# Optimization experiments

Hardware: AMD Instinct MI355X
Metric: run time of the kernel (lower is better)

Reference implementation:

```python
import jax, jax.numpy as jnp
import numpy as np

N, E, G = 30000, 480000, 64
IN, H, L = 24, 512, 6


def setup_inputs() -> dict:
    key = jax.random.key(0)
    ks = jax.random.split(key, 20)
    s = 0.05
    inp = {
        "x": jax.random.normal(ks[0], (N, IN), dtype=jnp.float32),
        "edge_index": jax.random.randint(ks[1], (2, E), 0, N, dtype=jnp.int64),
        "batch": jnp.sort(jax.random.randint(ks[2], (N,), 0, G, dtype=jnp.int64)),
        # node encoder
        "enc_w": jax.random.normal(ks[3], (IN, H), dtype=jnp.float32) * s,
        "enc_b": jnp.zeros((H,), dtype=jnp.float32),
        # per-layer message MLP (stacked over L layers), weights stored [in, out]
        "mlp_w1": jax.random.normal(ks[4], (L, H, H), dtype=jnp.float32) * s,
        "mlp_b1": jnp.zeros((L, H), dtype=jnp.float32),
        "mlp_w2": jax.random.normal(ks[5], (L, H, H), dtype=jnp.float32) * s,
        "mlp_b2": jnp.zeros((L, H), dtype=jnp.float32),
        # per-layer GRUCell params, [in, 3H] layout (gates order: r, z, n)
        "gru_wih": jax.random.normal(ks[6], (L, H, 3 * H), dtype=jnp.float32) * s,
        "gru_whh": jax.random.normal(ks[7], (L, H, 3 * H), dtype=jnp.float32) * s,
        "gru_bih": jnp.zeros((L, 3 * H), dtype=jnp.float32),
        "gru_bhh": jnp.zeros((L, 3 * H), dtype=jnp.float32),
        # head MLP
        "head_w1": jax.random.normal(ks[8], (H, H // 2), dtype=jnp.float32) * s,
        "head_b1": jnp.zeros((H // 2,), dtype=jnp.float32),
        "head_w2": jax.random.normal(ks[9], (H // 2, 1), dtype=jnp.float32) * s,
        "head_b2": jnp.zeros((1,), dtype=jnp.float32),
    }
    return inp


def _forward(x, edge_index, batch, enc_w, enc_b, mlp_w1, mlp_b1, mlp_w2, mlp_b2,
             gru_wih, gru_whh, gru_bih, gru_bhh, head_w1, head_b1, head_w2, head_b2):
    src, dst = edge_index[0], edge_index[1]
    h = x @ enc_w + enc_b  # [N, H]
    for l in range(L):
        # message MLP depends only on x_j, so compute per-node then gather
        msg = jnp.maximum(h @ mlp_w1[l] + mlp_b1[l], 0.0) @ mlp_w2[l] + mlp_b2[l]  # [N, H]
        # scatter-add over edges + self-loop contribution (add_self_loops)
        m = jax.ops.segment_sum(msg[src], dst, num_segments=N) + msg  # [N, H]
        # GRUCell(input=m, hidden=h); torch gate order: reset, update, new
        gi = m @ gru_wih[l] + gru_bih[l]
        gh = h @ gru_whh[l] + gru_bhh[l]
        r = jax.nn.sigmoid(gi[:, :H] + gh[:, :H])
        z = jax.nn.sigmoid(gi[:, H:2 * H] + gh[:, H:2 * H])
        n = jnp.tanh(gi[:, 2 * H:] + r * gh[:, 2 * H:])
        h = (1.0 - z) * n + z * h
    # global mean pool per graph
    sums = jax.ops.segment_sum(h, batch, num_segments=G)
    cnt = jax.ops.segment_sum(jnp.ones((N,), dtype=h.dtype), batch, num_segments=G)
    pooled = sums / jnp.maximum(cnt, 1.0)[:, None]  # [G, H]
    out = jnp.maximum(pooled @ head_w1 + head_b1, 0.0) @ head_w2 + head_b2
    return out[:, 0]  # [G]


def reference(x, edge_index, batch, enc_w, enc_b, mlp_w1, mlp_b1, mlp_w2, mlp_b2,
              gru_wih, gru_whh, gru_bih, gru_bhh, head_w1, head_b1, head_w2, head_b2):
    return _forward(x, edge_index, batch, enc_w, enc_b, mlp_w1, mlp_b1, mlp_w2, mlp_b2,
                    gru_wih, gru_whh, gru_bih, gru_bhh, head_w1, head_b1, head_w2, head_b2)
```

## Files before the change

### kernel.cpp

```cpp
#include <hip/hip_runtime.h>
#include <hip/hip_bf16.h>
#include <math.h>

#define N_NODES 30000
#define N_EDGES 480000
#define N_GRAPH 64
#define DIN 24
#define HD 512
#define NL 6

typedef __hip_bfloat16 bf16;
using short8 = __attribute__((ext_vector_type(8))) short;
using f32x4 = __attribute__((ext_vector_type(4))) float;

#define ASYNC16(gp, lp)                                              \
    __builtin_amdgcn_global_load_lds(                                \
        (const __attribute__((address_space(1))) void*)(gp),         \
        (__attribute__((address_space(3))) void*)(lp), 16, 0, 0)

__device__ __forceinline__ float sigmoidf_(float x) { return 1.0f / (1.0f + expf(-x)); }
__device__ __forceinline__ float b2f(unsigned short u) {
    return __uint_as_float(((unsigned int)u) << 16);
}
__device__ __forceinline__ unsigned short f2b(float f) {
    bf16 b = __float2bfloat16(f);
    return *(unsigned short*)&b;
}

__global__ __launch_bounds__(256) void enc_kernel(const float* __restrict__ x,
                                                  const float* __restrict__ w,
                                                  const float* __restrict__ b,
                                                  bf16* __restrict__ h) {
    __shared__ float xs[DIN];
    int row = blockIdx.x;
    int tid = threadIdx.x;
    if (tid < DIN) xs[tid] = x[row * DIN + tid];
    __syncthreads();
    for (int c = tid; c < HD; c += 256) {
        float acc = b[c];
#pragma unroll
        for (int k = 0; k < DIN; k++) acc = fmaf(xs[k], w[k * HD + c], acc);
        h[(size_t)row * HD + c] = __float2bfloat16(acc);
    }
}

__global__ __launch_bounds__(256) void twcvt_kernel(const float* __restrict__ W,
                                                    bf16* __restrict__ WtH,
                                                    bf16* __restrict__ WtL, int Nc) {
    __shared__ float s[32][33];
    int l = blockIdx.z;
    const float* Wp = W + (size_t)l * HD * Nc;
    size_t ob = (size_t)l * HD * Nc;
    int k0 = blockIdx.y * 32, c0 = blockIdx.x * 32;
    int tx = threadIdx.x & 31, ty = threadIdx.x >> 5;
    for (int r = ty; r < 32; r += 8) s[r][tx] = Wp[(size_t)(k0 + r) * Nc + c0 + tx];
    __syncthreads();
    for (int r = ty; r < 32; r += 8) {
        float v = s[tx][r];
        unsigned short hu = f2b(v);
        float hf = b2f(hu);
        size_t o = ob + (size_t)(c0 + r) * HD + k0 + tx;
        *(unsigned short*)&WtH[o] = hu;
        WtL[o] = __float2bfloat16(v - hf);
    }
}

template <bool RELU>
__global__ __launch_bounds__(256) void gemm_mfma(const bf16* __restrict__ A,
                                                 const bf16* __restrict__ WtH,
                                                 const bf16* __restrict__ WtL,
                                                 const float* __restrict__ bias,
                                                 bf16* __restrict__ C, int n) {
    __shared__ bf16 As[128 * 32];
    __shared__ bf16 BH[128 * 32];
    __shared__ bf16 BL[128 * 32];
    int tid = threadIdx.x;
    int wv = tid >> 6, lane = tid & 63;
    int quad = lane >> 4, l16 = lane & 15;
    int crow = lane >> 2, cseg = lane & 3;
    int gseg = cseg ^ ((crow >> 1) & 3);
    int fsw = (quad ^ ((l16 >> 1) & 3)) * 8;
    int row0 = blockIdx.y * 128, col0 = blockIdx.x * 128;
    f32x4 acc[2][8] = {};

    int aoff[4], alds[4];
    int boff[8];
    const bf16* wb = (wv == 2) ? WtH : WtL;
    bf16* bdst = (wv == 2) ? BH : BL;
    if (wv < 2) {
#pragma unroll
        for (int j = 0; j < 4; j++) {
            int ch = wv * 4 + j;
            int gr = row0 + ch * 16 + crow;
            if (gr > n - 1) gr = n - 1;
            aoff[j] = gr * HD + gseg * 8;
            alds[j] = ch * 512;
        }
    } else {
#pragma unroll
        for (int s = 0; s < 8; s++) boff[s] = (col0 + s * 16 + crow) * HD + gseg * 8;
    }

    for (int kt = 0; kt < 512; kt += 32) {
        if (wv < 2) {
#pragma unroll
            for (int j = 0; j < 4; j++) ASYNC16(&A[aoff[j] + kt], &As[alds[j]]);
        } else {
#pragma unroll
            for (int s = 0; s < 8; s++) ASYNC16(&wb[boff[s] + kt], &bdst[s * 512]);
        }
        __syncthreads();
        short8 af[2];
#pragma unroll
        for (int i = 0; i < 2; i++)
            af[i] = *(const short8*)&As[(wv * 32 + i * 16 + l16) * 32 + fsw];
#pragma unroll
        for (int t = 0; t < 8; t++) {
            int fo = (t * 16 + l16) * 32 + fsw;
            short8 bh = *(const short8*)&BH[fo];
            short8 bl = *(const short8*)&BL[fo];
#pragma unroll
            for (int i = 0; i < 2; i++) {
                acc[i][t] = __builtin_amdgcn_mfma_f32_16x16x32_bf16(af[i], bh, acc[i][t], 0, 0, 0);
                acc[i][t] = __builtin_amdgcn_mfma_f32_16x16x32_bf16(af[i], bl, acc[i][t], 0, 0, 0);
            }
        }
        __syncthreads();
    }
#pragma unroll
    for (int t = 0; t < 8; t++) {
        int col = col0 + t * 16 + l16;
        float bb = bias[col];
#pragma unroll
        for (int i = 0; i < 2; i++) {
#pragma unroll
            for (int r = 0; r < 4; r++) {
                int row = row0 + wv * 32 + i * 16 + quad * 4 + r;
                if (row < n) {
                    float v = acc[i][t][r] + bb;
                    if (RELU) v = fmaxf(v, 0.0f);
                    C[(size_t)row * HD + col] = __float2bfloat16(v);
                }
            }
        }
    }
}

__global__ __launch_bounds__(256, 2) void gru_mfma(const bf16* __restrict__ M,
                                                   const bf16* __restrict__ Hc,
                                                   const bf16* __restrict__ WiH,
                                                   const bf16* __restrict__ WiL,
                                                   const bf16* __restrict__ WhH,
                                                   const bf16* __restrict__ WhL,
                                                   const float* __restrict__ bih,
                                                   const float* __restrict__ bhh,
                                                   bf16* __restrict__ Hn, int n) {
    __shared__ bf16 Ms[128 * 32];
    __shared__ bf16 Hs[128 * 32];
    __shared__ bf16 Ws[12 * 64 * 32];
    int tid = threadIdx.x;
    int wv = tid >> 6, lane = tid & 63;
    int quad = lane >> 4, l16 = lane & 15;
    int crow = lane >> 2, cseg = lane & 3;
    int gseg = cseg ^ ((crow >> 1) & 3);
    int fsw = (quad ^ ((l16 >> 1) & 3)) * 8;
    int row0 = blockIdx.y * 128, col0 = blockIdx.x * 64;
    f32x4 aR[2][4] = {}, aZ[2][4] = {}, aI[2][4] = {}, aHn[2][4] = {};

    int moff[8];
    const bf16* wgp[4];
    int wlds[4];
    if (wv == 0) {
#pragma unroll
        for (int j = 0; j < 8; j++) {
            int gr = row0 + j * 16 + crow;
            if (gr > n - 1) gr = n - 1;
            moff[j] = gr * HD + gseg * 8;
        }
    } else {
        const bf16* wbase[4] = {WiH, WiL, WhH, WhL};
#pragma unroll
        for (int pp = 0; pp < 4; pp++) {
            int p = (wv - 1) * 4 + pp;
            int mat = (p >= 6);
            int q = p - mat * 6;
            int g = q >> 1, pl = q & 1;
            const bf16* base = wbase[mat * 2 + pl] + (size_t)(g * HD + col0) * HD;
            wgp[pp] = base + crow * HD + gseg * 8;
            wlds[pp] = p * 2048;
        }
    }

    for (int kt = 0; kt < 512; kt += 32) {
        if (wv == 0) {
#pragma unroll
            for (int j = 0; j < 8; j++) {
                ASYNC16(&M[moff[j] + kt], &Ms[j * 512]);
                ASYNC16(&Hc[moff[j] + kt], &Hs[j * 512]);
            }
        } else {
#pragma unroll
            for (int pp = 0; pp < 4; pp++)
#pragma unroll
                for (int s = 0; s < 4; s++)
                    ASYNC16(wgp[pp] + (size_t)s * 16 * HD + kt, &Ws[wlds[pp] + s * 512]);
        }
        __syncthreads();
        short8 am[2], ah[2];
#pragma unroll
        for (int i = 0; i < 2; i++) {
            am[i] = *(const short8*)&Ms[(wv * 32 + i * 16 + l16) * 32 + fsw];
            ah[i] = *(const short8*)&Hs[(wv * 32 + i * 16 + l16) * 32 + fsw];
        }
#pragma unroll
        for (int t = 0; t < 4; t++) {
            int fo = (t * 16 + l16) * 32 + fsw;
            short8 wrh = *(const short8*)&Ws[0 * 2048 + fo];
            short8 wrl = *(const short8*)&Ws[1 * 2048 + fo];
            short8 wzh = *(const short8*)&Ws[2 * 2048 + fo];
            short8 wzl = *(const short8*)&Ws[3 * 2048 + fo];
            short8 wnh = *(const short8*)&Ws[4 * 2048 + fo];
            short8 wnl = *(const short8*)&Ws[5 * 2048 + fo];
            short8 vrh = *(const short8*)&Ws[6 * 2048 + fo];
            short8 vrl = *(const short8*)&Ws[7 * 2048 + fo];
            short8 vzh = *(const short8*)&Ws[8 * 2048 + fo];
            short8 vzl = *(const short8*)&Ws[9 * 2048 + fo];
            short8 vnh = *(const short8*)&Ws[10 * 2048 + fo];
            short8 vnl = *(const short8*)&Ws[11 * 2048 + fo];
#pragma unroll
            for (int i = 0; i < 2; i++) {
                aR[i][t] = __builtin_amdgcn_mfma_f32_16x16x32_bf16(am[i], wrh, aR[i][t], 0, 0, 0);
                aR[i][t] = __builtin_amdgcn_mfma_f32_16x16x32_bf16(am[i], wrl, aR[i][t], 0, 0, 0);
                aR[i][t] = __builtin_amdgcn_mfma_f32_16x16x32_bf16(ah[i], vrh, aR[i][t], 0, 0, 0);
                aR[i][t] = __builtin_amdgcn_mfma_f32_16x16x32_bf16(ah[i], vrl, aR[i][t], 0, 0, 0);
                aZ[i][t] = __builtin_amdgcn_mfma_f32_16x16x32_bf16(am[i], wzh, aZ[i][t], 0, 0, 0);
                aZ[i][t] = __builtin_amdgcn_mfma_f32_16x16x32_bf16(am[i], wzl, aZ[i][t], 0, 0, 0);
                aZ[i][t] = __builtin_amdgcn_mfma_f32_16x16x32_bf16(ah[i], vzh, aZ[i][t], 0, 0, 0);
                aZ[i][t] = __builtin_amdgcn_mfma_f32_16x16x32_bf16(ah[i], vzl, aZ[i][t], 0, 0, 0);
                aI[i][t] = __builtin_amdgcn_mfma_f32_16x16x32_bf16(am[i], wnh, aI[i][t], 0, 0, 0);
                aI[i][t] = __builtin_amdgcn_mfma_f32_16x16x32_bf16(am[i], wnl, aI[i][t], 0, 0, 0);
                aHn[i][t] = __builtin_amdgcn_mfma_f32_16x16x32_bf16(ah[i], vnh, aHn[i][t], 0, 0, 0);
                aHn[i][t] = __builtin_amdgcn_mfma_f32_16x16x32_bf16(ah[i], vnl, aHn[i][t], 0, 0, 0);
            }
        }
        __syncthreads();
    }
    const unsigned short* hp = (const unsigned short*)Hc;
#pragma unroll
    for (int t = 0; t < 4; t++) {
        int col = col0 + t * 16 + l16;
        float brz = bih[col] + bhh[col];
        float bzz = bih[HD + col] + bhh[HD + col];
        float bin_ = bih[2 * HD + col];
        float bhn_ = bhh[2 * HD + col];
#pragma unroll
        for (int i = 0; i < 2; i++) {
#pragma unroll
            for (int r = 0; r < 4; r++) {
                int row = row0 + wv * 32 + i * 16 + quad * 4 + r;
                if (row < n) {
                    float rg = sigmoidf_(aR[i][t][r] + brz);
                    float zg = sigmoidf_(aZ[i][t][r] + bzz);
                    float ng = tanhf(aI[i][t][r] + bin_ + rg * (aHn[i][t][r] + bhn_));
                    float hold = b2f(hp[(size_t)row * HD + col]);
                    Hn[(size_t)row * HD + col] = __float2bfloat16((1.0f - zg) * ng + zg * hold);
                }
            }
        }
    }
}

__global__ __launch_bounds__(256) void deg_kernel(const int* __restrict__ dst,
                                                  int* __restrict__ deg) {
    int e = blockIdx.x * 256 + threadIdx.x;
    if (e < N_EDGES) atomicAdd(&deg[dst[e]], 1);
}

__global__ __launch_bounds__(1024) void scan_kernel(const int* __restrict__ deg,
                                                    int* __restrict__ offs) {
    __shared__ int buf[1024];
    __shared__ int carry_s;
    int tid = threadIdx.x;
    if (tid == 0) carry_s = 0;
    __syncthreads();
    for (int base = 0; base < N_NODES; base += 1024) {
        int v = (base + tid < N_NODES) ? deg[base + tid] : 0;
        buf[tid] = v;
        __syncthreads();
        for (int s = 1; s < 1024; s <<= 1) {
            int t = (tid >= s) ? buf[tid - s] : 0;
            __syncthreads();
            buf[tid] += t;
            __syncthreads();
        }
        int incl = buf[tid];
        if (base + tid < N_NODES) offs[base + tid] = carry_s + incl - v;
        __syncthreads();
        if (tid == 0) carry_s += buf[1023];
        __syncthreads();
    }
    if (tid == 0) offs[N_NODES] = carry_s;
}

__global__ __launch_bounds__(256) void bucket_kernel(const int* __restrict__ src,
                                                     const int* __restrict__ dst,
                                                     const int* __restrict__ offs,
                                                     int* __restrict__ cursor,
                                                     unsigned short* __restrict__ elist) {
    int e = blockIdx.x * 256 + threadIdx.x;
    if (e >= N_EDGES) return;
    int d = dst[e];
    int pos = atomicAdd(&cursor[d], 1);
    elist[offs[d] + pos] = (unsigned short)src[e];
}

__global__ __launch_bounds__(256) void gather_kernel(const bf16* __restrict__ msg,
                                                     bf16* __restrict__ m,
                                                     const unsigned short* __restrict__ elist,
                                                     const int* __restrict__ offs) {
    int nid = blockIdx.x, tid = threadIdx.x;
    int beg = offs[nid], end = offs[nid + 1];
    const unsigned int* mp = (const unsigned int*)msg;
    unsigned int u = mp[(size_t)nid * 256 + tid];
    float ax = b2f((unsigned short)(u & 0xffffu));
    float ay = b2f((unsigned short)(u >> 16));
    int e = beg;
    for (; e + 3 < end; e += 4) {
        unsigned int v0 = mp[(size_t)elist[e] * 256 + tid];
        unsigned int v1 = mp[(size_t)elist[e + 1] * 256 + tid];
        unsigned int v2 = mp[(size_t)elist[e + 2] * 256 + tid];
        unsigned int v3 = mp[(size_t)elist[e + 3] * 256 + tid];
        ax += b2f((unsigned short)(v0 & 0xffffu)) + b2f((unsigned short)(v1 & 0xffffu)) +
              b2f((unsigned short)(v2 & 0xffffu)) + b2f((unsigned short)(v3 & 0xffffu));
        ay += b2f((unsigned short)(v0 >> 16)) + b2f((unsigned short)(v1 >> 16)) +
              b2f((unsigned short)(v2 >> 16)) + b2f((unsigned short)(v3 >> 16));
    }
    for (; e < end; e++) {
        unsigned int v0 = mp[(size_t)elist[e] * 256 + tid];
        ax += b2f((unsigned short)(v0 & 0xffffu));
        ay += b2f((unsigned short)(v0 >> 16));
    }
    unsigned int out = ((unsigned int)f2b(ay) << 16) | (unsigned int)f2b(ax);
    ((unsigned int*)m)[(size_t)nid * 256 + tid] = out;
}

__global__ __launch_bounds__(256) void pool_kernel(const bf16* __restrict__ h,
                                                   const int* __restrict__ batch,
                                                   float* __restrict__ pooled,
                                                   float* __restrict__ cnt) {
    int g = blockIdx.x;
    int col = blockIdx.y * 256 + threadIdx.x;
    int lo = 0, hi = N_NODES;
    while (lo < hi) { int mid = (lo + hi) >> 1; if (batch[mid] < g) lo = mid + 1; else hi = mid; }
    int gs = lo;
    hi = N_NODES;
    while (lo < hi) { int mid = (lo + hi) >> 1; if (batch[mid] < g + 1) lo = mid + 1; else hi = mid; }
    int ge = lo;
    const unsigned short* hp = (const unsigned short*)h;
    float acc = 0.0f;
    int r = gs;
    for (; r + 3 < ge; r += 4) {
        acc += b2f(hp[(size_t)r * HD + col]) + b2f(hp[(size_t)(r + 1) * HD + col]) +
               b2f(hp[(size_t)(r + 2) * HD + col]) + b2f(hp[(size_t)(r + 3) * HD + col]);
    }
    for (; r < ge; r++) acc += b2f(hp[(size_t)r * HD + col]);
    pooled[g * HD + col] = acc;
    if (blockIdx.y == 0 && threadIdx.x == 0) cnt[g] = (float)(ge - gs);
}

__global__ __launch_bounds__(256) void head_kernel(const float* __restrict__ pooled,
                                                   const float* __restrict__ cnt,
                                                   const float* __restrict__ w1,
                                                   const float* __restrict__ b1,
                                                   const float* __restrict__ w2,
                                                   const float* __restrict__ b2,
                                                   float* __restrict__ out) {
    __shared__ float prow[HD];
    __shared__ float red[256];
    int g = blockIdx.x, tid = threadIdx.x;
    float c = fmaxf(cnt[g], 1.0f);
    for (int j = tid; j < HD; j += 256) prow[j] = pooled[g * HD + j] / c;
    __syncthreads();
    float acc = b1[tid];
    for (int k = 0; k < HD; k++) acc = fmaf(prow[k], w1[k * 256 + tid], acc);
    red[tid] = fmaxf(acc, 0.0f) * w2[tid];
    __syncthreads();
    for (int s = 128; s > 0; s >>= 1) {
        if (tid < s) red[tid] += red[tid + s];
        __syncthreads();
    }
    if (tid == 0) out[g] = red[0] + b2[0];
}

extern "C" void kernel_launch(void* const* d_in, const int* in_sizes, int n_in,
                              void* d_out, int out_size, void* d_ws, size_t ws_size,
                              hipStream_t stream) {
    const float* x = (const float*)d_in[0];
    const int* eidx = (const int*)d_in[1];
    const int* batch = (const int*)d_in[2];
    const float* enc_w = (const float*)d_in[3];
    const float* enc_b = (const float*)d_in[4];
    const float* mlp_w1 = (const float*)d_in[5];
    const float* mlp_b1 = (const float*)d_in[6];
    const float* mlp_w2 = (const float*)d_in[7];
    const float* mlp_b2 = (const float*)d_in[8];
    const float* gru_wih = (const float*)d_in[9];
    const float* gru_whh = (const float*)d_in[10];
    const float* gru_bih = (const float*)d_in[11];
    const float* gru_bhh = (const float*)d_in[12];
    const float* head_w1 = (const float*)d_in[13];
    const float* head_b1 = (const float*)d_in[14];
    const float* head_w2 = (const float*)d_in[15];
    const float* head_b2 = (const float*)d_in[16];
    const int* src = eidx;
    const int* dst = eidx + N_EDGES;

    const size_t NH = (size_t)N_NODES * HD;
    char* p = (char*)d_ws;
    auto alloc = [&](size_t bytes) { char* q = p; p += (bytes + 255) & ~(size_t)255; return q; };
    bf16* S0 = (bf16*)alloc(NH * 2);
    bf16* S1 = (bf16*)alloc(NH * 2);
    bf16* S2 = (bf16*)alloc(NH * 2);
    bf16* w1tH = (bf16*)alloc((size_t)NL * HD * HD * 2);
    bf16* w1tL = (bf16*)alloc((size_t)NL * HD * HD * 2);
    bf16* w2tH = (bf16*)alloc((size_t)NL * HD * HD * 2);
    bf16* w2tL = (bf16*)alloc((size_t)NL * HD * HD * 2);
    bf16* wihtH = (bf16*)alloc((size_t)NL * 3 * HD * HD * 2);
    bf16* wihtL = (bf16*)alloc((size_t)NL * 3 * HD * HD * 2);
    bf16* whhtH = (bf16*)alloc((size_t)NL * 3 * HD * HD * 2);
    bf16* whhtL = (bf16*)alloc((size_t)NL * 3 * HD * HD * 2);
    float* pooled = (float*)alloc((size_t)N_GRAPH * HD * 4);
    float* cnt = (float*)alloc(N_GRAPH * 4);
    int* deg = (int*)alloc((N_NODES + 1) * 4);
    int* offs = (int*)alloc((N_NODES + 1) * 4);
    unsigned short* elist = (unsigned short*)alloc((size_t)N_EDGES * 2);

    twcvt_kernel<<<dim3(16, 16, NL), 256, 0, stream>>>(mlp_w1, w1tH, w1tL, HD);
    twcvt_kernel<<<dim3(16, 16, NL), 256, 0, stream>>>(mlp_w2, w2tH, w2tL, HD);
    twcvt_kernel<<<dim3(48, 16, NL), 256, 0, stream>>>(gru_wih, wihtH, wihtL, 3 * HD);
    twcvt_kernel<<<dim3(48, 16, NL), 256, 0, stream>>>(gru_whh, whhtH, whhtL, 3 * HD);

    hipMemsetAsync(deg, 0, (N_NODES + 1) * sizeof(int), stream);
    deg_kernel<<<(N_EDGES + 255) / 256, 256, 0, stream>>>(dst, deg);
    scan_kernel<<<1, 1024, 0, stream>>>(deg, offs);
    hipMemsetAsync(deg, 0, (N_NODES + 1) * sizeof(int), stream);
    bucket_kernel<<<(N_EDGES + 255) / 256, 256, 0, stream>>>(src, dst, offs, deg, elist);

    enc_kernel<<<N_NODES, 256, 0, stream>>>(x, enc_w, enc_b, S0);

    bf16* hcur = S0;
    bf16* hoth = S1;
    dim3 ggrid(4, (N_NODES + 127) / 128);
    dim3 ugrid(8, (N_NODES + 127) / 128);

    for (int l = 0; l < NL; l++) {
        size_t wsq = (size_t)l * HD * HD;
        size_t wgq = (size_t)l * 3 * HD * HD;
        const float* b1 = mlp_b1 + (size_t)l * HD;
        const float* b2 = mlp_b2 + (size_t)l * HD;
        const float* bih = gru_bih + (size_t)l * 3 * HD;
        const float* bhh = gru_bhh + (size_t)l * 3 * HD;

        gemm_mfma<true><<<ggrid, 256, 0, stream>>>(hcur, w1tH + wsq, w1tL + wsq, b1, hoth, N_NODES);
        gemm_mfma<false><<<ggrid, 256, 0, stream>>>(hoth, w2tH + wsq, w2tL + wsq, b2, S2, N_NODES);
        gather_kernel<<<N_NODES, 256, 0, stream>>>(S2, hoth, elist, offs);
        gru_mfma<<<ugrid, 256, 0, stream>>>(hoth, hcur, wihtH + wgq, wihtL + wgq,
                                            whhtH + wgq, whhtL + wgq, bih, bhh, S2, N_NODES);
        bf16* newh = S2;
        S2 = hcur;
        hcur = newh;
    }

    pool_kernel<<<dim3(N_GRAPH, 2), 256, 0, stream>>>(hcur, batch, pooled, cnt);
    head_kernel<<<N_GRAPH, 256, 0, stream>>>(pooled, cnt, head_w1, head_b1, head_w2, head_b2,
                                             (float*)d_out);
}
```

Baseline: 2.823 ms.

## Load activation fragments directly from global memory instead of staging in LDS

In both the MLP GEMM and the GRU GEMM, the A-side operands (activations, M and H) are now read straight from global memory into registers as MFMA fragments rather than copied asynchronously into shared memory first. Only the weight tiles still go through LDS, and their loading is spread evenly across all four waves. The lower LDS footprint lets the launch bounds raise the occupancy targets (4 and 3 blocks per CU). In exchange, each wave issues uncoalesced 16-byte global loads per row, and the load latency sits before the barrier without any pipelining.

```diff
diff --git a/kernel.cpp b/kernel.cpp
--- a/kernel.cpp
+++ b/kernel.cpp
@@ -66,12 +66,11 @@
 }
 
 template <bool RELU>
-__global__ __launch_bounds__(256) void gemm_mfma(const bf16* __restrict__ A,
-                                                 const bf16* __restrict__ WtH,
-                                                 const bf16* __restrict__ WtL,
-                                                 const float* __restrict__ bias,
-                                                 bf16* __restrict__ C, int n) {
-    __shared__ bf16 As[128 * 32];
+__global__ __launch_bounds__(256, 4) void gemm_mfma(const bf16* __restrict__ A,
+                                                    const bf16* __restrict__ WtH,
+                                                    const bf16* __restrict__ WtL,
+                                                    const float* __restrict__ bias,
+                                                    bf16* __restrict__ C, int n) {
     __shared__ bf16 BH[128 * 32];
     __shared__ bf16 BL[128 * 32];
     int tid = threadIdx.x;
@@ -83,37 +82,27 @@
     int row0 = blockIdx.y * 128, col0 = blockIdx.x * 128;
     f32x4 acc[2][8] = {};
 
-    int aoff[4], alds[4];
-    int boff[8];
-    const bf16* wb = (wv == 2) ? WtH : WtL;
-    bf16* bdst = (wv == 2) ? BH : BL;
-    if (wv < 2) {
-#pragma unroll
-        for (int j = 0; j < 4; j++) {
-            int ch = wv * 4 + j;
-            int gr = row0 + ch * 16 + crow;
-            if (gr > n - 1) gr = n - 1;
-            aoff[j] = gr * HD + gseg * 8;
-            alds[j] = ch * 512;
-        }
-    } else {
-#pragma unroll
-        for (int s = 0; s < 8; s++) boff[s] = (col0 + s * 16 + crow) * HD + gseg * 8;
-    }
+    int arow[2];
+#pragma unroll
+    for (int i = 0; i < 2; i++) {
+        int r = row0 + wv * 32 + i * 16 + l16;
+        arow[i] = (r < n) ? r : (n - 1);
+    }
+    const bf16* wb = (wv >= 2) ? WtL : WtH;
+    bf16* bdst = (wv >= 2) ? BL : BH;
+    int ch0 = (wv & 1) * 4;
+    int boff[4];
+#pragma unroll
+    for (int s = 0; s < 4; s++) boff[s] = (col0 + (ch0 + s) * 16 + crow) * HD + gseg * 8;
 
     for (int kt = 0; kt < 512; kt += 32) {
-        if (wv < 2) {
-#pragma unroll
-            for (int j = 0; j < 4; j++) ASYNC16(&A[aoff[j] + kt], &As[alds[j]]);
-        } else {
-#pragma unroll
-            for (int s = 0; s < 8; s++) ASYNC16(&wb[boff[s] + kt], &bdst[s * 512]);
-        }
-        __syncthreads();
+#pragma unroll
+        for (int s = 0; s < 4; s++) ASYNC16(&wb[boff[s] + kt], &bdst[(ch0 + s) * 512]);
         short8 af[2];
 #pragma unroll
         for (int i = 0; i < 2; i++)
-            af[i] = *(const short8*)&As[(wv * 32 + i * 16 + l16) * 32 + fsw];
+            af[i] = *(const short8*)&A[(size_t)arow[i] * HD + kt + quad * 8];
+        __syncthreads();
 #pragma unroll
         for (int t = 0; t < 8; t++) {
             int fo = (t * 16 + l16) * 32 + fsw;
@@ -146,7 +135,7 @@
     }
 }
 
-__global__ __launch_bounds__(256, 2) void gru_mfma(const bf16* __restrict__ M,
+__global__ __launch_bounds__(256, 3) void gru_mfma(const bf16* __restrict__ M,
                                                    const bf16* __restrict__ Hc,
                                                    const bf16* __restrict__ WiH,
                                                    const bf16* __restrict__ WiL,
@@ -155,8 +144,6 @@
                                                    const float* __restrict__ bih,
                                                    const float* __restrict__ bhh,
                                                    bf16* __restrict__ Hn, int n) {
-    __shared__ bf16 Ms[128 * 32];
-    __shared__ bf16 Hs[128 * 32];
     __shared__ bf16 Ws[12 * 64 * 32];
     int tid = threadIdx.x;
     int wv = tid >> 6, lane = tid & 63;
@@ -167,51 +154,39 @@
     int row0 = blockIdx.y * 128, col0 = blockIdx.x * 64;
     f32x4 aR[2][4] = {}, aZ[2][4] = {}, aI[2][4] = {}, aHn[2][4] = {};
 
-    int moff[8];
-    const bf16* wgp[4];
-    int wlds[4];
-    if (wv == 0) {
-#pragma unroll
-        for (int j = 0; j < 8; j++) {
-            int gr = row0 + j * 16 + crow;
-            if (gr > n - 1) gr = n - 1;
-            moff[j] = gr * HD + gseg * 8;
-        }
-    } else {
-        const bf16* wbase[4] = {WiH, WiL, WhH, WhL};
-#pragma unroll
-        for (int pp = 0; pp < 4; pp++) {
-            int p = (wv - 1) * 4 + pp;
-            int mat = (p >= 6);
-            int q = p - mat * 6;
-            int g = q >> 1, pl = q & 1;
-            const bf16* base = wbase[mat * 2 + pl] + (size_t)(g * HD + col0) * HD;
-            wgp[pp] = base + crow * HD + gseg * 8;
-            wlds[pp] = p * 2048;
-        }
+    int arow[2];
+#pragma unroll
+    for (int i = 0; i < 2; i++) {
+        int r = row0 + wv * 32 + i * 16 + l16;
+        arow[i] = (r < n) ? r : (n - 1);
+    }
+    const bf16* wbase[4] = {WiH, WiL, WhH, WhL};
+    const bf16* wgp[3];
+    int wlds[3];
+#pragma unroll
+    for (int pp = 0; pp < 3; pp++) {
+        int p = wv * 3 + pp;
+        int mat = (p >= 6);
+        int q = p - mat * 6;
+        int g = q >> 1, pl = q & 1;
+        const bf16* base = wbase[mat * 2 + pl] + (size_t)(g * HD + col0) * HD;
+        wgp[pp] = base + crow * HD + gseg * 8;
+        wlds[pp] = p * 2048;
     }
 
     for (int kt = 0; kt < 512; kt += 32) {
-        if (wv == 0) {
-#pragma unroll
-            for (int j = 0; j < 8; j++) {
-                ASYNC16(&M[moff[j] + kt], &Ms[j * 512]);
-                ASYNC16(&Hc[moff[j] + kt], &Hs[j * 512]);
-            }
-        } else {
-#pragma unroll
-            for (int pp = 0; pp < 4; pp++)
-#pragma unroll
-                for (int s = 0; s < 4; s++)
-                    ASYNC16(wgp[pp] + (size_t)s * 16 * HD + kt, &Ws[wlds[pp] + s * 512]);
-        }
-        __syncthreads();
+#pragma unroll
+        for (int pp = 0; pp < 3; pp++)
+#pragma unroll
+            for (int s = 0; s < 4; s++)
+                ASYNC16(wgp[pp] + (size_t)s * 16 * HD + kt, &Ws[wlds[pp] + s * 512]);
         short8 am[2], ah[2];
 #pragma unroll
         for (int i = 0; i < 2; i++) {
-            am[i] = *(const short8*)&Ms[(wv * 32 + i * 16 + l16) * 32 + fsw];
-            ah[i] = *(const short8*)&Hs[(wv * 32 + i * 16 + l16) * 32 + fsw];
-        }
+            am[i] = *(const short8*)&M[(size_t)arow[i] * HD + kt + quad * 8];
+            ah[i] = *(const short8*)&Hc[(size_t)arow[i] * HD + kt + quad * 8];
+        }
+        __syncthreads();
 #pragma unroll
         for (int t = 0; t < 4; t++) {
             int fo = (t * 16 + l16) * 32 + fsw;
```

After: 3.698 ms. 1.31x slower.
